# Kernel tuning notes

Hardware: AMD Instinct MI355X
Metric: run time of the kernel (lower is better)

The kernel has to match this reference:

```python
import jax, jax.numpy as jnp
import numpy as np

TEXT_DIM = 768
IMAGE_DIM = 1024
HIDDEN = 2048
FF = 128
HEADS = 8
HEAD_DIM = HIDDEN // HEADS  # 256


def setup_inputs() -> dict:
    key = jax.random.key(0)
    ks = jax.random.split(key, 16)
    def lin(k, fan_in, fan_out):
        bound = 1.0 / np.sqrt(fan_in)
        kw, kb = jax.random.split(k)
        W = jax.random.uniform(kw, (fan_in, fan_out), jnp.float32, -bound, bound)
        b = jax.random.uniform(kb, (fan_out,), jnp.float32, -bound, bound)
        return W, b
    text = jax.random.normal(ks[0], (16, 512, TEXT_DIM), jnp.float32)
    image = jax.random.normal(ks[1], (16, 576, IMAGE_DIM), jnp.float32)
    wq, bq = lin(ks[2], TEXT_DIM, HIDDEN)
    wk, bk = lin(ks[3], IMAGE_DIM, HIDDEN)
    wv, bv = lin(ks[4], IMAGE_DIM, HIDDEN)
    wr, br = lin(ks[5], HIDDEN, TEXT_DIM)
    w1, b1 = lin(ks[6], TEXT_DIM, FF)
    w2, b2 = lin(ks[7], FF, TEXT_DIM)
    gamma = jnp.ones((TEXT_DIM,), jnp.float32)
    beta = jnp.zeros((TEXT_DIM,), jnp.float32)
    return {"text": text, "image": image,
            "wq": wq, "bq": bq, "wk": wk, "bk": bk, "wv": wv, "bv": bv,
            "wr": wr, "br": br, "w1": w1, "b1": b1, "w2": w2, "b2": b2,
            "gamma": gamma, "beta": beta}


def reference(text, image, wq, bq, wk, bk, wv, bv, wr, br, w1, b1, w2, b2, gamma, beta):
    # Dropout is identity (eval mode).
    bs, lt, _ = text.shape
    li = image.shape[1]
    Q = (text @ wq + bq).reshape(bs, lt, HEADS, HEAD_DIM)
    K = (image @ wk + bk).reshape(bs, li, HEADS, HEAD_DIM)
    V = (image @ wv + bv).reshape(bs, li, HEADS, HEAD_DIM)
    scale = jnp.sqrt(jnp.float32(HEAD_DIM))
    scores = jnp.einsum('bqhd,bkhd->bhqk', Q, K) / scale  # [B,H,Lt,Li]
    attn = jax.nn.softmax(scores, axis=-1)
    x = jnp.einsum('bhqk,bkhd->bqhd', attn, V).reshape(bs, lt, HIDDEN)
    out = x @ wr + br  # [B,Lt,text_dim]
    ff = jax.nn.relu(out @ w1 + b1) @ w2 + b2
    out = out + ff
    # LayerNorm over last dim (eps=1e-5, torch default)
    mu = jnp.mean(out, axis=-1, keepdims=True)
    var = jnp.mean(jnp.square(out - mu), axis=-1, keepdims=True)
    return (out - mu) / jnp.sqrt(var + 1e-5) * gamma + beta
```

## Files before the change

kernel.cpp:

```cpp
#include <hip/hip_runtime.h>
#include <stdint.h>
#include <stddef.h>

typedef __attribute__((ext_vector_type(8))) short bf16x8;
typedef __attribute__((ext_vector_type(4))) float f32x4;

typedef __attribute__((address_space(1))) unsigned int uint_g;
typedef __attribute__((address_space(3))) unsigned int uint_l;

#define DEV static __device__ __forceinline__

DEV unsigned short f2bf(float f) {
  unsigned int u = __float_as_uint(f);
  u += 0x7FFFu + ((u >> 16) & 1u);
  return (unsigned short)(u >> 16);
}

DEV void gl_lds16(const unsigned short* g, unsigned short* l) {
  __builtin_amdgcn_global_load_lds((const uint_g*)g, (uint_l*)l, 16, 0, 0);
}

__global__ __launch_bounds__(256) void k_f32_to_bf16(const float* __restrict__ in,
                                                     unsigned short* __restrict__ out, int n4) {
  int i = blockIdx.x * 256 + threadIdx.x;
  if (i >= n4) return;
  const float4 v = ((const float4*)in)[i];
  ushort4 o;
  o.x = f2bf(v.x); o.y = f2bf(v.y); o.z = f2bf(v.z); o.w = f2bf(v.w);
  ((ushort4*)out)[i] = o;
}

__global__ __launch_bounds__(256) void k_transpose_to_bf16(const float* __restrict__ in,
                                                           unsigned short* __restrict__ out,
                                                           int R, int C) {
  __shared__ unsigned short tile[32][33];
  const int c0 = blockIdx.x << 5, r0 = blockIdx.y << 5;
  const int tx = threadIdx.x & 31, ty = threadIdx.x >> 5;
  #pragma unroll
  for (int i = 0; i < 32; i += 8)
    tile[ty + i][tx] = f2bf(in[(size_t)(r0 + ty + i) * C + c0 + tx]);
  __syncthreads();
  #pragma unroll
  for (int i = 0; i < 32; i += 8)
    out[(size_t)(c0 + ty + i) * R + r0 + tx] = tile[tx][ty + i];
}

enum { EPI_BIAS = 0, EPI_VT = 3, EPI_DUAL = 4, EPI_RELU = 5, EPI_RES = 6 };

template <int BM, int BN, int EPI>
__global__ __launch_bounds__(256)
void k_gemm(const unsigned short* __restrict__ A, const unsigned short* __restrict__ B,
            int lda, int ldb, int kSteps,
            void* C0, void* C1, const float* bias, const float* resid, int ldc, float scale) {
  constexpr int TM = BM / 32;
  constexpr int TN = BN / 32;
  __shared__ unsigned short At[2][BM * 32];
  __shared__ unsigned short Bt[2][BN * 32];

  const int t = threadIdx.x;
  const int lane = t & 63, wave = t >> 6;
  const int wm = wave >> 1, wn = wave & 1;

  const unsigned short* Ab = A + (size_t)blockIdx.y * BM * lda;
  const unsigned short* Bb = B + (size_t)blockIdx.x * BN * ldb;

  const int frow = lane & 15, fk = (lane >> 4) << 3;

  f32x4 acc[TM][TN] = {};

  auto stage = [&](int ks, int bi) {
    const int k0 = ks << 5;
    #pragma unroll
    for (int r = 0; r < BM / 64; ++r) {
      int off16 = (r << 8) + t;
      int row = off16 >> 2, kk = (off16 & 3) << 3;
      gl_lds16(Ab + (size_t)row * lda + k0 + kk, &At[bi][(row << 5) + kk]);
    }
    #pragma unroll
    for (int r = 0; r < BN / 64; ++r) {
      int off16 = (r << 8) + t;
      int row = off16 >> 2, kk = (off16 & 3) << 3;
      gl_lds16(Bb + (size_t)row * ldb + k0 + kk, &Bt[bi][(row << 5) + kk]);
    }
  };

  stage(0, 0);

  for (int ks = 0; ks < kSteps; ++ks) {
    const int buf = ks & 1;
    __syncthreads();
    if (ks + 1 < kSteps) stage(ks + 1, buf ^ 1);

    bf16x8 af[TM], bv[TN];
    #pragma unroll
    for (int mi = 0; mi < TM; ++mi)
      af[mi] = *(const bf16x8*)&At[buf][((wm * (BM / 2) + mi * 16 + frow) << 5) + fk];
    #pragma unroll
    for (int ni = 0; ni < TN; ++ni)
      bv[ni] = *(const bf16x8*)&Bt[buf][((wn * (BN / 2) + ni * 16 + frow) << 5) + fk];
    #pragma unroll
    for (int mi = 0; mi < TM; ++mi)
      #pragma unroll
      for (int ni = 0; ni < TN; ++ni)
        acc[mi][ni] = __builtin_amdgcn_mfma_f32_16x16x32_bf16(af[mi], bv[ni], acc[mi][ni], 0, 0, 0);
  }

  const int mb = blockIdx.y * BM + wm * (BM / 2) + ((lane >> 4) << 2);
  const int nb = blockIdx.x * BN + wn * (BN / 2) + (lane & 15);

  #pragma unroll
  for (int mi = 0; mi < TM; ++mi) {
    const int m = mb + mi * 16;
    #pragma unroll
    for (int ni = 0; ni < TN; ++ni) {
      const int n = nb + ni * 16;
      f32x4 v = acc[mi][ni];
      if constexpr (EPI == EPI_BIAS) {
        unsigned short* O = (unsigned short*)C0;
        const float bv2 = bias[n];
        #pragma unroll
        for (int r = 0; r < 4; ++r) O[(size_t)(m + r) * ldc + n] = f2bf((v[r] + bv2) * scale);
      } else if constexpr (EPI == EPI_VT) {
        const int b = m / 576, li = m - b * 576;
        const int h = n >> 8, d = n & 255;
        const float bv2 = bias[n];
        ushort4 o;
        o.x = f2bf(v[0] + bv2); o.y = f2bf(v[1] + bv2);
        o.z = f2bf(v[2] + bv2); o.w = f2bf(v[3] + bv2);
        *(ushort4*)((unsigned short*)C0 + ((size_t)((b * 8 + h) * 256 + d)) * 576 + li) = o;
      } else if constexpr (EPI == EPI_DUAL) {
        float* Of = (float*)C0;
        unsigned short* Ob = (unsigned short*)C1;
        const float bv2 = bias[n];
        #pragma unroll
        for (int r = 0; r < 4; ++r) {
          const float x = v[r] + bv2;
          const size_t idx = (size_t)(m + r) * ldc + n;
          Of[idx] = x; Ob[idx] = f2bf(x);
        }
      } else if constexpr (EPI == EPI_RELU) {
        unsigned short* O = (unsigned short*)C0;
        const float bv2 = bias[n];
        #pragma unroll
        for (int r = 0; r < 4; ++r) {
          const float x = v[r] + bv2;
          O[(size_t)(m + r) * ldc + n] = f2bf(x > 0.f ? x : 0.f);
        }
      } else if constexpr (EPI == EPI_RES) {
        float* Of = (float*)C0;
        const float bv2 = bias[n];
        #pragma unroll
        for (int r = 0; r < 4; ++r) {
          const size_t idx = (size_t)(m + r) * ldc + n;
          Of[idx] = v[r] + bv2 + resid[idx];
        }
      }
    }
  }
}

__global__ __launch_bounds__(512, 2)
void k_flash(const unsigned short* __restrict__ Q, const unsigned short* __restrict__ K,
             const unsigned short* __restrict__ Vt, unsigned short* __restrict__ X) {
  __shared__ unsigned short Ks[2][8 * 32 * 32];
  __shared__ unsigned short Vs[2][256 * 32];
  __shared__ unsigned short Ps[256 * 40];
  __shared__ unsigned short Ones[512];

  const int t = threadIdx.x, lane = t & 63, w = t >> 6;
  const int frow = lane & 15, quad = lane >> 4, fk = quad << 3;

  const int id = blockIdx.x;
  const int qb = (id >> 3) & 1;
  const int bh = (id & 7) | ((id >> 4) << 3);
  const int b = bh >> 3, h = bh & 7;
  const int q0 = qb << 8;

  const unsigned short* Kg = K + ((size_t)b * 576) * 2048 + h * 256;
  const unsigned short* Vg = Vt + (size_t)bh * 147456;

  Ones[t] = (t < 32) ? (unsigned short)0x3F80 : (unsigned short)0;

  bf16x8 Qf[2][8];
  #pragma unroll
  for (int half = 0; half < 2; ++half) {
    const unsigned short* Qg =
        Q + ((size_t)(b * 512 + q0 + w * 32 + half * 16 + frow)) * 2048 + h * 256;
    #pragma unroll
    for (int kd = 0; kd < 8; ++kd)
      Qf[half][kd] = *(const bf16x8*)(Qg + kd * 32 + fk);
  }

  f32x4 acc_o[2][17] = {};

  auto stage = [&](int s, int bi) {
    const int li0 = s << 5;
    unsigned short* Kb = &Ks[bi][0];
    unsigned short* Vb = &Vs[bi][0];
    #pragma unroll
    for (int it = 0; it < 2; ++it) {
      int e = (it << 9) + t;
      int row = e >> 2, c = (e & 3) << 3;
      int kd = row >> 5, li = row & 31;
      gl_lds16(Kg + (size_t)(li0 + li) * 2048 + kd * 32 + c, &Kb[(row << 5) + c]);
    }
    #pragma unroll
    for (int it = 0; it < 2; ++it) {
      int e = (it << 9) + t;
      int d = e >> 2, c = (e & 3) << 3;
      gl_lds16(Vg + (size_t)d * 576 + li0 + c, &Vb[(d << 5) + c]);
    }
  };

  stage(0, 0);

  const int prow = (w << 5) + (quad << 2);

  for (int s = 0; s < 18; ++s) {
    const int buf = s & 1;
    __syncthreads();
    if (s + 1 < 18) stage(s + 1, buf ^ 1);

    f32x4 acc_s[2][2] = {};
    #pragma unroll
    for (int kd = 0; kd < 8; ++kd) {
      #pragma unroll
      for (int ni = 0; ni < 2; ++ni) {
        const bf16x8 bv = *(const bf16x8*)&Ks[buf][((kd * 32 + ni * 16 + frow) << 5) + fk];
        acc_s[0][ni] = __builtin_amdgcn_mfma_f32_16x16x32_bf16(Qf[0][kd], bv, acc_s[0][ni], 0, 0, 0);
        acc_s[1][ni] = __builtin_amdgcn_mfma_f32_16x16x32_bf16(Qf[1][kd], bv, acc_s[1][ni], 0, 0, 0);
      }
    }

    #pragma unroll
    for (int half = 0; half < 2; ++half)
      #pragma unroll
      for (int ni = 0; ni < 2; ++ni)
        #pragma unroll
        for (int r = 0; r < 4; ++r)
          Ps[(prow + half * 16 + r) * 40 + ni * 16 + frow] =
              f2bf(__builtin_amdgcn_exp2f(acc_s[half][ni][r]));

    bf16x8 paf[2];
    paf[0] = *(const bf16x8*)&Ps[((w << 5) + frow) * 40 + fk];
    paf[1] = *(const bf16x8*)&Ps[((w << 5) + 16 + frow) * 40 + fk];
    #pragma unroll
    for (int ni = 0; ni < 16; ++ni) {
      const bf16x8 bv = *(const bf16x8*)&Vs[buf][((ni * 16 + frow) << 5) + fk];
      acc_o[0][ni] = __builtin_amdgcn_mfma_f32_16x16x32_bf16(paf[0], bv, acc_o[0][ni], 0, 0, 0);
      acc_o[1][ni] = __builtin_amdgcn_mfma_f32_16x16x32_bf16(paf[1], bv, acc_o[1][ni], 0, 0, 0);
    }
    {
      const bf16x8 bv = *(const bf16x8*)&Ones[(frow << 5) + fk];
      acc_o[0][16] = __builtin_amdgcn_mfma_f32_16x16x32_bf16(paf[0], bv, acc_o[0][16], 0, 0, 0);
      acc_o[1][16] = __builtin_amdgcn_mfma_f32_16x16x32_bf16(paf[1], bv, acc_o[1][16], 0, 0, 0);
    }
  }

  #pragma unroll
  for (int half = 0; half < 2; ++half) {
    float linv[4];
    #pragma unroll
    for (int r = 0; r < 4; ++r)
      linv[r] = 1.0f / __shfl(acc_o[half][16][r], lane & 48);
    unsigned short* Xo = X + ((size_t)(b * 512 + q0 + w * 32 + half * 16 + (quad << 2))) * 2048 +
                         h * 256 + frow;
    #pragma unroll
    for (int ni = 0; ni < 16; ++ni)
      #pragma unroll
      for (int r = 0; r < 4; ++r)
        Xo[(size_t)r * 2048 + ni * 16] = f2bf(acc_o[half][ni][r] * linv[r]);
  }
}

__global__ __launch_bounds__(256) void k_layernorm768(float* O, const float* __restrict__ gamma,
                                                      const float* __restrict__ beta) {
  const int row = blockIdx.x;
  float* p = O + (size_t)row * 768;
  const int t = threadIdx.x;
  const int lane = t & 63, wave = t >> 6;
  const float x0 = p[t], x1 = p[t + 256], x2 = p[t + 512];
  float s = x0 + x1 + x2;
  float q = x0 * x0 + x1 * x1 + x2 * x2;
  #pragma unroll
  for (int i = 32; i >= 1; i >>= 1) { s += __shfl_xor(s, i); q += __shfl_xor(q, i); }
  __shared__ float rs[4], rq[4];
  if (lane == 0) { rs[wave] = s; rq[wave] = q; }
  __syncthreads();
  s = rs[0] + rs[1] + rs[2] + rs[3];
  q = rq[0] + rq[1] + rq[2] + rq[3];
  const float mu = s * (1.0f / 768.0f);
  const float var = q * (1.0f / 768.0f) - mu * mu;
  const float inv = rsqrtf(var + 1e-5f);
  p[t]       = (x0 - mu) * inv * gamma[t]       + beta[t];
  p[t + 256] = (x1 - mu) * inv * gamma[t + 256] + beta[t + 256];
  p[t + 512] = (x2 - mu) * inv * gamma[t + 512] + beta[t + 512];
}

extern "C" void kernel_launch(void* const* d_in, const int* in_sizes, int n_in,
                              void* d_out, int out_size, void* d_ws, size_t ws_size,
                              hipStream_t stream) {
  const float* text  = (const float*)d_in[0];
  const float* image = (const float*)d_in[1];
  const float* wq = (const float*)d_in[2];  const float* bq = (const float*)d_in[3];
  const float* wk = (const float*)d_in[4];  const float* bk = (const float*)d_in[5];
  const float* wv = (const float*)d_in[6];  const float* bv = (const float*)d_in[7];
  const float* wr = (const float*)d_in[8];  const float* br = (const float*)d_in[9];
  const float* w1 = (const float*)d_in[10]; const float* b1 = (const float*)d_in[11];
  const float* w2 = (const float*)d_in[12]; const float* b2 = (const float*)d_in[13];
  const float* gamma = (const float*)d_in[14]; const float* beta = (const float*)d_in[15];

  uint8_t* ws = (uint8_t*)d_ws;
  constexpr size_t o_Tbf = 0;
  constexpr size_t o_Ibf = 12582912;
  constexpr size_t o_X   = 0;
  constexpr size_t o_Q   = 33554432;
  constexpr size_t o_Kb  = o_Q   + 33554432;
  constexpr size_t o_Vt  = o_Kb  + 37748736;
  constexpr size_t o_wqT = o_Vt  + 37748736;
  constexpr size_t o_wkT = o_wqT + 3145728;
  constexpr size_t o_wvT = o_wkT + 4194304;
  constexpr size_t o_wrT = o_wvT + 4194304;
  constexpr size_t o_w1T = o_wrT + 3145728;
  constexpr size_t o_w2T = o_w1T + 196608;
  constexpr size_t o_OutB= o_w2T + 196608;
  constexpr size_t o_H   = o_OutB+ 12582912;

  unsigned short* Tbf  = (unsigned short*)(ws + o_Tbf);
  unsigned short* Ibf  = (unsigned short*)(ws + o_Ibf);
  unsigned short* Xb   = (unsigned short*)(ws + o_X);
  unsigned short* Qb   = (unsigned short*)(ws + o_Q);
  unsigned short* Kb   = (unsigned short*)(ws + o_Kb);
  unsigned short* Vt   = (unsigned short*)(ws + o_Vt);
  unsigned short* wqT  = (unsigned short*)(ws + o_wqT);
  unsigned short* wkT  = (unsigned short*)(ws + o_wkT);
  unsigned short* wvT  = (unsigned short*)(ws + o_wvT);
  unsigned short* wrT  = (unsigned short*)(ws + o_wrT);
  unsigned short* w1T  = (unsigned short*)(ws + o_w1T);
  unsigned short* w2T  = (unsigned short*)(ws + o_w2T);
  unsigned short* OutB = (unsigned short*)(ws + o_OutB);
  unsigned short* Hb   = (unsigned short*)(ws + o_H);
  float* OutF = (float*)d_out;

  const dim3 blk(256);

  k_f32_to_bf16<<<dim3(6144), blk, 0, stream>>>(text,  Tbf, 1572864);
  k_f32_to_bf16<<<dim3(9216), blk, 0, stream>>>(image, Ibf, 2359296);
  k_transpose_to_bf16<<<dim3(64, 24), blk, 0, stream>>>(wq, wqT, 768, 2048);
  k_transpose_to_bf16<<<dim3(64, 32), blk, 0, stream>>>(wk, wkT, 1024, 2048);
  k_transpose_to_bf16<<<dim3(64, 32), blk, 0, stream>>>(wv, wvT, 1024, 2048);
  k_transpose_to_bf16<<<dim3(24, 64), blk, 0, stream>>>(wr, wrT, 2048, 768);
  k_transpose_to_bf16<<<dim3(4, 24),  blk, 0, stream>>>(w1, w1T, 768, 128);
  k_transpose_to_bf16<<<dim3(24, 4),  blk, 0, stream>>>(w2, w2T, 128, 768);

  k_gemm<128, 128, EPI_BIAS><<<dim3(16, 64), blk, 0, stream>>>(
      Tbf, wqT, 768, 768, 24, Qb, nullptr, bq, nullptr, 2048, 0.0625f * 1.44269504f);
  k_gemm<128, 128, EPI_BIAS><<<dim3(16, 72), blk, 0, stream>>>(
      Ibf, wkT, 1024, 1024, 32, Kb, nullptr, bk, nullptr, 2048, 1.0f);
  k_gemm<128, 128, EPI_VT><<<dim3(16, 72), blk, 0, stream>>>(
      Ibf, wvT, 1024, 1024, 32, Vt, nullptr, bv, nullptr, 0, 1.0f);

  k_flash<<<dim3(256), dim3(512), 0, stream>>>(Qb, Kb, Vt, Xb);

  k_gemm<128, 128, EPI_DUAL><<<dim3(6, 64), blk, 0, stream>>>(
      Xb, wrT, 2048, 2048, 64, OutF, OutB, br, nullptr, 768, 1.0f);

  k_gemm<64, 64, EPI_RELU><<<dim3(2, 128), blk, 0, stream>>>(
      OutB, w1T, 768, 768, 24, Hb, nullptr, b1, nullptr, 128, 1.0f);

  k_gemm<128, 128, EPI_RES><<<dim3(6, 64), blk, 0, stream>>>(
      Hb, w2T, 128, 128, 4, OutF, nullptr, b2, (const float*)d_out, 768, 1.0f);

  k_layernorm768<<<dim3(8192), blk, 0, stream>>>(OutF, gamma, beta);

  (void)in_sizes; (void)n_in; (void)out_size; (void)ws_size;
}
```

Measured before the change: 472.8 us.

## Add 256x256 eight-wave pipelined GEMM for Q/K/V projections

Adds a new GEMM kernel with 256x256 tiles, 512 threads, BK=64, XOR-swizzled LDS, and direct global-to-LDS loads. Its main loop is split into four MFMA phases, with the next tile's loads interleaved between them, explicit waitcnt/barrier placement, and setprio around the MFMA bursts. The Q, K and V projection GEMMs now use this kernel in place of the 128x128 tile kernel. The aim is more data reuse per tile and better overlap of memory with compute. The cost is 128KB of LDS per block and fewer blocks in flight (256/288 per GEMM).

```diff
diff --git a/kernel.cpp b/kernel.cpp
--- a/kernel.cpp
+++ b/kernel.cpp
@@ -46,6 +46,163 @@
 }
 
 enum { EPI_BIAS = 0, EPI_VT = 3, EPI_DUAL = 4, EPI_RELU = 5, EPI_RES = 6 };
+
+template <int EPI>
+__global__ __launch_bounds__(512, 2)
+void k_gemm8(const unsigned short* __restrict__ A, const unsigned short* __restrict__ B,
+             int lda, int ldb, int kTiles,
+             void* C0, const float* bias, int ldc, float scale) {
+  __shared__ unsigned short As[2][256 * 64];
+  __shared__ unsigned short Bs[2][256 * 64];
+
+  const int t = threadIdx.x;
+  const int lane = t & 63, w = t >> 6;
+  const int wm = w >> 2, wn = w & 3;
+  const int frow = lane & 15, quad = lane >> 4;
+
+  const unsigned short* Ab = A + (size_t)blockIdx.y * 256 * lda;
+  const unsigned short* Bb = B + (size_t)blockIdx.x * 256 * ldb;
+
+  f32x4 acc[8][4] = {};
+
+  auto stA = [&](int kt, int bi, int h) {
+    #pragma unroll
+    for (int it = 0; it < 2; ++it) {
+      int e = (it << 9) + t;
+      int row = (h << 7) + (e >> 3);
+      int c16 = (e & 7) ^ (row & 7);
+      gl_lds16(Ab + (size_t)row * lda + (kt << 6) + (c16 << 3),
+               &As[bi][(row << 6) + ((e & 7) << 3)]);
+    }
+  };
+  auto stB = [&](int kt, int bi, int h) {
+    #pragma unroll
+    for (int it = 0; it < 2; ++it) {
+      int e = (it << 9) + t;
+      int row = (h << 7) + (e >> 3);
+      int c16 = (e & 7) ^ (row & 7);
+      gl_lds16(Bb + (size_t)row * ldb + (kt << 6) + (c16 << 3),
+               &Bs[bi][(row << 6) + ((e & 7) << 3)]);
+    }
+  };
+  auto frag = [&](const unsigned short* buf, int row, int ksl) -> bf16x8 {
+    int col = ((ksl << 5) + (quad << 3)) ^ ((row & 7) << 3);
+    return *(const bf16x8*)&buf[(row << 6) + col];
+  };
+
+  stB(0, 0, 0); stB(0, 0, 1); stA(0, 0, 0); stA(0, 0, 1);
+  if (kTiles > 1) { stB(1, 1, 0); stB(1, 1, 1); stA(1, 1, 0); }
+
+  bf16x8 a[4][2], b0[2][2], b1[2][2];
+  const int arow = wm << 7, brow = wn << 6;
+
+  for (int kt = 0; kt < kTiles; ++kt) {
+    const int pb = kt & 1, qb = pb ^ 1;
+    const unsigned short* Ac = As[pb];
+    const unsigned short* Bc = Bs[pb];
+
+    if (kt + 1 < kTiles) {
+      stA(kt + 1, qb, 1);
+      asm volatile("s_waitcnt vmcnt(8)" ::: "memory");
+    } else {
+      asm volatile("s_waitcnt vmcnt(0)" ::: "memory");
+    }
+    asm volatile("s_barrier" ::: "memory");
+    #pragma unroll
+    for (int m = 0; m < 4; ++m)
+      #pragma unroll
+      for (int k = 0; k < 2; ++k) a[m][k] = frag(Ac, arow + (m << 4) + frow, k);
+    #pragma unroll
+    for (int n = 0; n < 2; ++n)
+      #pragma unroll
+      for (int k = 0; k < 2; ++k) b0[n][k] = frag(Bc, brow + (n << 4) + frow, k);
+    asm volatile("s_waitcnt lgkmcnt(0)" ::: "memory");
+    __builtin_amdgcn_s_setprio(1);
+    #pragma unroll
+    for (int m = 0; m < 4; ++m)
+      #pragma unroll
+      for (int n = 0; n < 2; ++n)
+        #pragma unroll
+        for (int k = 0; k < 2; ++k)
+          acc[m][n] = __builtin_amdgcn_mfma_f32_16x16x32_bf16(a[m][k], b0[n][k], acc[m][n], 0, 0, 0);
+    __builtin_amdgcn_s_setprio(0);
+    asm volatile("s_barrier" ::: "memory");
+
+    #pragma unroll
+    for (int n = 0; n < 2; ++n)
+      #pragma unroll
+      for (int k = 0; k < 2; ++k) b1[n][k] = frag(Bc, brow + 32 + (n << 4) + frow, k);
+    asm volatile("s_barrier" ::: "memory");
+    asm volatile("s_waitcnt lgkmcnt(0)" ::: "memory");
+    __builtin_amdgcn_s_setprio(1);
+    #pragma unroll
+    for (int m = 0; m < 4; ++m)
+      #pragma unroll
+      for (int n = 0; n < 2; ++n)
+        #pragma unroll
+        for (int k = 0; k < 2; ++k)
+          acc[m][2 + n] = __builtin_amdgcn_mfma_f32_16x16x32_bf16(a[m][k], b1[n][k], acc[m][2 + n], 0, 0, 0);
+    __builtin_amdgcn_s_setprio(0);
+    asm volatile("s_barrier" ::: "memory");
+
+    #pragma unroll
+    for (int m = 0; m < 4; ++m)
+      #pragma unroll
+      for (int k = 0; k < 2; ++k) a[m][k] = frag(Ac, arow + 64 + (m << 4) + frow, k);
+    if (kt + 2 < kTiles) stB(kt + 2, pb, 0);
+    asm volatile("s_barrier" ::: "memory");
+    asm volatile("s_waitcnt lgkmcnt(0)" ::: "memory");
+    __builtin_amdgcn_s_setprio(1);
+    #pragma unroll
+    for (int m = 0; m < 4; ++m)
+      #pragma unroll
+      for (int n = 0; n < 2; ++n)
+        #pragma unroll
+        for (int k = 0; k < 2; ++k)
+          acc[4 + m][n] = __builtin_amdgcn_mfma_f32_16x16x32_bf16(a[m][k], b0[n][k], acc[4 + m][n], 0, 0, 0);
+    __builtin_amdgcn_s_setprio(0);
+    asm volatile("s_barrier" ::: "memory");
+
+    if (kt + 2 < kTiles) { stB(kt + 2, pb, 1); stA(kt + 2, pb, 0); }
+    asm volatile("s_barrier" ::: "memory");
+    __builtin_amdgcn_s_setprio(1);
+    #pragma unroll
+    for (int m = 0; m < 4; ++m)
+      #pragma unroll
+      for (int n = 0; n < 2; ++n)
+        #pragma unroll
+        for (int k = 0; k < 2; ++k)
+          acc[4 + m][2 + n] = __builtin_amdgcn_mfma_f32_16x16x32_bf16(a[m][k], b1[n][k], acc[4 + m][2 + n], 0, 0, 0);
+    __builtin_amdgcn_s_setprio(0);
+    asm volatile("s_barrier" ::: "memory");
+  }
+
+  const int mb = blockIdx.y * 256 + wm * 128 + (quad << 2);
+  const int nb = blockIdx.x * 256 + wn * 64 + frow;
+  #pragma unroll
+  for (int mi = 0; mi < 8; ++mi) {
+    const int m = mb + mi * 16;
+    #pragma unroll
+    for (int ni = 0; ni < 4; ++ni) {
+      const int n = nb + ni * 16;
+      f32x4 v = acc[mi][ni];
+      if constexpr (EPI == EPI_BIAS) {
+        unsigned short* O = (unsigned short*)C0;
+        const float bv2 = bias[n];
+        #pragma unroll
+        for (int r = 0; r < 4; ++r) O[(size_t)(m + r) * ldc + n] = f2bf((v[r] + bv2) * scale);
+      } else if constexpr (EPI == EPI_VT) {
+        const int b = m / 576, li = m - b * 576;
+        const int h = n >> 8, d = n & 255;
+        const float bv2 = bias[n];
+        ushort4 o;
+        o.x = f2bf(v[0] + bv2); o.y = f2bf(v[1] + bv2);
+        o.z = f2bf(v[2] + bv2); o.w = f2bf(v[3] + bv2);
+        *(ushort4*)((unsigned short*)C0 + ((size_t)((b * 8 + h) * 256 + d)) * 576 + li) = o;
+      }
+    }
+  }
+}
 
 template <int BM, int BN, int EPI>
 __global__ __launch_bounds__(256)
@@ -120,14 +277,6 @@
         const float bv2 = bias[n];
         #pragma unroll
         for (int r = 0; r < 4; ++r) O[(size_t)(m + r) * ldc + n] = f2bf((v[r] + bv2) * scale);
-      } else if constexpr (EPI == EPI_VT) {
-        const int b = m / 576, li = m - b * 576;
-        const int h = n >> 8, d = n & 255;
-        const float bv2 = bias[n];
-        ushort4 o;
-        o.x = f2bf(v[0] + bv2); o.y = f2bf(v[1] + bv2);
-        o.z = f2bf(v[2] + bv2); o.w = f2bf(v[3] + bv2);
-        *(ushort4*)((unsigned short*)C0 + ((size_t)((b * 8 + h) * 256 + d)) * 576 + li) = o;
       } else if constexpr (EPI == EPI_DUAL) {
         float* Of = (float*)C0;
         unsigned short* Ob = (unsigned short*)C1;
@@ -353,12 +502,12 @@
   k_transpose_to_bf16<<<dim3(4, 24),  blk, 0, stream>>>(w1, w1T, 768, 128);
   k_transpose_to_bf16<<<dim3(24, 4),  blk, 0, stream>>>(w2, w2T, 128, 768);
 
-  k_gemm<128, 128, EPI_BIAS><<<dim3(16, 64), blk, 0, stream>>>(
-      Tbf, wqT, 768, 768, 24, Qb, nullptr, bq, nullptr, 2048, 0.0625f * 1.44269504f);
-  k_gemm<128, 128, EPI_BIAS><<<dim3(16, 72), blk, 0, stream>>>(
-      Ibf, wkT, 1024, 1024, 32, Kb, nullptr, bk, nullptr, 2048, 1.0f);
-  k_gemm<128, 128, EPI_VT><<<dim3(16, 72), blk, 0, stream>>>(
-      Ibf, wvT, 1024, 1024, 32, Vt, nullptr, bv, nullptr, 0, 1.0f);
+  k_gemm8<EPI_BIAS><<<dim3(8, 32), dim3(512), 0, stream>>>(
+      Tbf, wqT, 768, 768, 12, Qb, bq, 2048, 0.0625f * 1.44269504f);
+  k_gemm8<EPI_BIAS><<<dim3(8, 36), dim3(512), 0, stream>>>(
+      Ibf, wkT, 1024, 1024, 16, Kb, bk, 2048, 1.0f);
+  k_gemm8<EPI_VT><<<dim3(8, 36), dim3(512), 0, stream>>>(
+      Ibf, wvT, 1024, 1024, 16, Vt, bv, 0, 1.0f);
 
   k_flash<<<dim3(256), dim3(512), 0, stream>>>(Qb, Kb, Vt, Xb);
 
```

New measurement: 505.8 us. 1.07x slower.
